# Kernel optimization log

Measured on AMD Instinct MI355X. Metric: run time of the kernel, lower is better.

The kernel has to match this reference:

```python
import jax, jax.numpy as jnp
import numpy as np

T = 2048        # sequence length
E = 1024        # embedding_dim
H = 1024        # hidden_dim
V = 50257       # vocab_size
TAGS = 50       # tagset_size


def setup_inputs() -> dict:
    key = jax.random.key(0)
    ks = jax.random.split(key, 8)
    s = 1.0 / np.sqrt(H)
    return {
        "sentence": jax.random.randint(ks[0], (T,), 0, V, dtype=jnp.int64),
        "emb": jax.random.normal(ks[1], (V, E), dtype=jnp.float32),
        "W_ih": jax.random.uniform(ks[2], (3 * H, E), jnp.float32, -s, s),
        "W_hh": jax.random.uniform(ks[3], (3 * H, H), jnp.float32, -s, s),
        "b_ih": jax.random.uniform(ks[4], (3 * H,), jnp.float32, -s, s),
        "b_hh": jax.random.uniform(ks[5], (3 * H,), jnp.float32, -s, s),
        "W_out": jax.random.uniform(ks[6], (TAGS, H), jnp.float32, -s, s),
        "b_out": jax.random.uniform(ks[7], (TAGS,), jnp.float32, -s, s),
    }


def _gru_scan(x, W_ih, W_hh, b_ih, b_hh):
    # x: [T, E]. Precompute all input-side gate projections in one GEMM.
    gi_all = x @ W_ih.T + b_ih            # [T, 3H]
    W_hhT = W_hh.T                         # [H, 3H]
    h0 = jnp.zeros((W_hh.shape[1],), x.dtype)

    def step(h, gi):
        gh = h @ W_hhT + b_hh              # [3H]
        i_r, i_z, i_n = jnp.split(gi, 3)
        h_r, h_z, h_n = jnp.split(gh, 3)
        r = jax.nn.sigmoid(i_r + h_r)
        z = jax.nn.sigmoid(i_z + h_z)
        n = jnp.tanh(i_n + r * h_n)
        h_new = (1.0 - z) * n + z * h
        return h_new, h_new

    _, hs = jax.lax.scan(step, h0, gi_all)  # hs: [T, H]
    return hs


def reference(sentence, emb, W_ih, W_hh, b_ih, b_hh, W_out, b_out):
    x = emb[sentence]                       # [T, E] embedding lookup
    hs = _gru_scan(x, W_ih, W_hh, b_ih, b_hh)  # [T, H]
    tag_space = hs @ W_out.T + b_out        # [T, TAGS]
    return jax.nn.log_softmax(tag_space, axis=-1)
```

## Files before the change

### kernel.cpp

```cpp
#include <hip/hip_runtime.h>
#include <hip/hip_bf16.h>


#define T_SEQ 2048
#define E_DIM 1024
#define H_DIM 1024
#define N3H   3072
#define VTAGS 50
#define VOCAB 50257
#define NWG   64
#define IPW   (H_DIM / NWG)
#define SBLK  512

typedef short bf16x8 __attribute__((ext_vector_type(8)));
typedef float f32x4  __attribute__((ext_vector_type(4)));
typedef unsigned int u32x4v __attribute__((ext_vector_type(4)));

__device__ inline unsigned short f2bf_rne(float f) {
  unsigned int u = __float_as_uint(f);
  u += 0x7FFFu + ((u >> 16) & 1u);
  return (unsigned short)(u >> 16);
}

__global__ __launch_bounds__(256) void k_gather_cast(
    const int* __restrict__ sent, const float* __restrict__ emb,
    unsigned short* __restrict__ Xb) {
  const int t = blockIdx.x;
  int row = sent[t];
  row = (row < 0) ? 0 : ((row >= VOCAB) ? VOCAB - 1 : row);
  const float4* src = (const float4*)(emb + (size_t)row * E_DIM);
  float4 v = src[threadIdx.x];
  ushort4 o;
  o.x = f2bf_rne(v.x); o.y = f2bf_rne(v.y); o.z = f2bf_rne(v.z); o.w = f2bf_rne(v.w);
  ((ushort4*)(Xb + (size_t)t * E_DIM))[threadIdx.x] = o;
}

__global__ __launch_bounds__(256) void k_cast_w(
    const float* __restrict__ W, unsigned short* __restrict__ Wb) {
  const int r = blockIdx.x;
  const float4* src = (const float4*)(W + (size_t)r * E_DIM);
  float4 v = src[threadIdx.x];
  ushort4 o;
  o.x = f2bf_rne(v.x); o.y = f2bf_rne(v.y); o.z = f2bf_rne(v.z); o.w = f2bf_rne(v.w);
  ((ushort4*)(Wb + (size_t)r * E_DIM))[threadIdx.x] = o;
}

__global__ __launch_bounds__(256) void k_gemm_gi(
    const unsigned short* __restrict__ Xb, const unsigned short* __restrict__ Wb,
    const float* __restrict__ b_ih, float* __restrict__ gi) {
  const int tid = threadIdx.x;
  const int lane = tid & 63;
  const int wv = tid >> 6;
  const int m_base = blockIdx.y * 128 + (wv & 1) * 64;
  const int n_base = blockIdx.x * 128 + (wv >> 1) * 64;
  const int lr = lane & 15;
  const int kq = (lane >> 4) * 8;
  f32x4 acc[4][4] = {};
  for (int k0 = 0; k0 < E_DIM; k0 += 32) {
    bf16x8 a[4], b[4];
#pragma unroll
    for (int mi = 0; mi < 4; ++mi)
      a[mi] = *(const bf16x8*)(Xb + (size_t)(m_base + mi * 16 + lr) * E_DIM + k0 + kq);
#pragma unroll
    for (int ni = 0; ni < 4; ++ni)
      b[ni] = *(const bf16x8*)(Wb + (size_t)(n_base + ni * 16 + lr) * E_DIM + k0 + kq);
#pragma unroll
    for (int mi = 0; mi < 4; ++mi)
#pragma unroll
      for (int ni = 0; ni < 4; ++ni)
        acc[mi][ni] = __builtin_amdgcn_mfma_f32_16x16x32_bf16(a[mi], b[ni], acc[mi][ni], 0, 0, 0);
  }
  const int row_q = (lane >> 4) * 4;
#pragma unroll
  for (int mi = 0; mi < 4; ++mi) {
#pragma unroll
    for (int ni = 0; ni < 4; ++ni) {
      const int col  = n_base + ni * 16 + lr;
      const int row0 = m_base + mi * 16 + row_q;
      const float bv = b_ih[col];
#pragma unroll
      for (int rr = 0; rr < 4; ++rr)
        gi[(size_t)(row0 + rr) * N3H + col] = acc[mi][ni][rr] + bv;
    }
  }
}

__global__ __launch_bounds__(SBLK) __attribute__((amdgpu_waves_per_eu(2, 2)))
void k_gru_scan(const float* __restrict__ W_hh, const float* __restrict__ b_hh,
                const float* __restrict__ gi, float* __restrict__ hs,
                unsigned long long* mb) {
  const int wg  = blockIdx.x;
  const int tid = threadIdx.x;
  const int row = tid >> 5;
  const int cg  = tid & 31;
  const int i   = wg * IPW + row;

  __shared__ float hsh[2][H_DIM];

  f32x4 w0[8], w1[8], w2[8];
  {
    const f32x4* p0 = (const f32x4*)(W_hh + (size_t)i * H_DIM);
    const f32x4* p1 = (const f32x4*)(W_hh + (size_t)(H_DIM + i) * H_DIM);
    const f32x4* p2 = (const f32x4*)(W_hh + (size_t)(2 * H_DIM + i) * H_DIM);
#pragma unroll
    for (int q = 0; q < 8; ++q) {
      w0[q] = p0[cg + q * 32];
      w1[q] = p1[cg + q * 32];
      w2[q] = p2[cg + q * 32];
      asm volatile("" : "+v"(w0[q]), "+v"(w1[q]), "+v"(w2[q]));
    }
  }
  const float bh0 = b_hh[i], bh1 = b_hh[H_DIM + i], bh2 = b_hh[2 * H_DIM + i];

  for (int t = 0; t < T_SEQ; ++t) {
    const float gir = gi[(size_t)t * N3H + i];
    const float giz = gi[(size_t)t * N3H + H_DIM + i];
    const float gin = gi[(size_t)t * N3H + 2 * H_DIM + i];

    {
      const unsigned long long* pb = mb + (size_t)(t & 1) * H_DIM + tid * 2;
      const unsigned tt = (unsigned)t;
      u32x4v p;
      int it = 0;
      while (true) {
        asm volatile("global_load_dwordx4 %0, %1, off sc0 sc1\n\ts_waitcnt vmcnt(0)"
                     : "=v"(p) : "v"(pb));
        if (__all((p[1] == tt) & (p[3] == tt)) || ++it > (1 << 16)) break;
      }
      *(float2*)&hsh[t & 1][tid * 2] =
          make_float2(__uint_as_float(p[0]), __uint_as_float(p[2]));
    }
    __syncthreads();

    const float* hb = hsh[t & 1];
    const f32x4* hb4 = (const f32x4*)hb;
    float a0 = 0.f, a1 = 0.f, a2 = 0.f;
#pragma unroll
    for (int q = 0; q < 8; ++q) {
      f32x4 hv = hb4[cg + q * 32];
      a0 = fmaf(w0[q][0], hv[0], a0); a0 = fmaf(w0[q][1], hv[1], a0);
      a0 = fmaf(w0[q][2], hv[2], a0); a0 = fmaf(w0[q][3], hv[3], a0);
      a1 = fmaf(w1[q][0], hv[0], a1); a1 = fmaf(w1[q][1], hv[1], a1);
      a1 = fmaf(w1[q][2], hv[2], a1); a1 = fmaf(w1[q][3], hv[3], a1);
      a2 = fmaf(w2[q][0], hv[0], a2); a2 = fmaf(w2[q][1], hv[1], a2);
      a2 = fmaf(w2[q][2], hv[2], a2); a2 = fmaf(w2[q][3], hv[3], a2);
    }
#pragma unroll
    for (int off = 16; off >= 1; off >>= 1) {
      a0 += __shfl_xor(a0, off, 64);
      a1 += __shfl_xor(a1, off, 64);
      a2 += __shfl_xor(a2, off, 64);
    }
    const float r = 1.f / (1.f + __expf(-(gir + a0 + bh0)));
    const float z = 1.f / (1.f + __expf(-(giz + a1 + bh1)));
    const float nx = gin + r * (a2 + bh2);
    const float e2 = __expf(-2.f * fabsf(nx));
    float n = (1.f - e2) / (1.f + e2);
    n = (nx < 0.f) ? -n : n;
    const float hold = hb[i];
    const float hnew = (1.f - z) * n + z * hold;

    if (cg == 0) {
      const unsigned long long pack =
          ((unsigned long long)(unsigned)(t + 1) << 32) |
          (unsigned long long)__float_as_uint(hnew);
      __hip_atomic_store(&mb[(size_t)((t + 1) & 1) * H_DIM + i], pack,
                         __ATOMIC_RELAXED, __HIP_MEMORY_SCOPE_AGENT);
      hs[(size_t)t * H_DIM + i] = hnew;
    }
  }
}

__global__ __launch_bounds__(256) void k_out(
    const float* __restrict__ hs, const float* __restrict__ W_out,
    const float* __restrict__ b_out, float* __restrict__ out) {
  const int t = blockIdx.x;
  const int tid = threadIdx.x;
  const int wv = tid >> 6, lane = tid & 63;
  __shared__ float xs[H_DIM];
  __shared__ float tagv[64];
  ((float4*)xs)[tid] = ((const float4*)(hs + (size_t)t * H_DIM))[tid];
  __syncthreads();
  for (int g = wv; g < VTAGS; g += 4) {
    const float4* wr = (const float4*)(W_out + (size_t)g * H_DIM);
    const float4* xr = (const float4*)xs;
    float s = 0.f;
#pragma unroll
    for (int q = 0; q < 4; ++q) {
      float4 a = wr[lane * 4 + q];
      float4 b = xr[lane * 4 + q];
      s += a.x * b.x + a.y * b.y + a.z * b.z + a.w * b.w;
    }
#pragma unroll
    for (int off = 1; off < 64; off <<= 1) s += __shfl_xor(s, off, 64);
    if (lane == 0) tagv[g] = s + b_out[g];
  }
  __syncthreads();
  if (tid < 64) {
    const float v = (tid < VTAGS) ? tagv[tid] : -1e30f;
    float m = v;
#pragma unroll
    for (int off = 1; off < 64; off <<= 1) m = fmaxf(m, __shfl_xor(m, off, 64));
    float e = (tid < VTAGS) ? __expf(v - m) : 0.f;
    float se = e;
#pragma unroll
    for (int off = 1; off < 64; off <<= 1) se += __shfl_xor(se, off, 64);
    const float lse = logf(se);
    if (tid < VTAGS) out[(size_t)t * VTAGS + tid] = v - m - lse;
  }
}

extern "C" void kernel_launch(void* const* d_in, const int* in_sizes, int n_in,
                              void* d_out, int out_size, void* d_ws, size_t ws_size,
                              hipStream_t stream) {
  const int* sent    = (const int*)d_in[0];
  const float* emb   = (const float*)d_in[1];
  const float* W_ih  = (const float*)d_in[2];
  const float* W_hh  = (const float*)d_in[3];
  const float* b_ih  = (const float*)d_in[4];
  const float* b_hh  = (const float*)d_in[5];
  const float* W_out = (const float*)d_in[6];
  const float* b_out = (const float*)d_in[7];
  float* out = (float*)d_out;

  char* ws = (char*)d_ws;
  const size_t OFF_GI = 0;
  const size_t OFF_B  = (size_t)T_SEQ * N3H * 4;
  const size_t OFF_XB = OFF_B;
  const size_t OFF_WB = OFF_B + (size_t)T_SEQ * E_DIM * 2;
  const size_t OFF_HS = OFF_B;
  const size_t OFF_MB = OFF_B + 10485760;
  const size_t NEED = OFF_MB + 2 * H_DIM * 8;
  if (ws_size < NEED) return;

  float* gi = (float*)(ws + OFF_GI);
  unsigned short* Xb = (unsigned short*)(ws + OFF_XB);
  unsigned short* Wb = (unsigned short*)(ws + OFF_WB);
  float* hs = (float*)(ws + OFF_HS);
  unsigned long long* mb = (unsigned long long*)(ws + OFF_MB);

  hipMemsetAsync(mb, 0, 2 * H_DIM * 8, stream);

  k_gather_cast<<<T_SEQ, 256, 0, stream>>>(sent, emb, Xb);
  k_cast_w<<<N3H, 256, 0, stream>>>(W_ih, Wb);
  k_gemm_gi<<<dim3(N3H / 128, T_SEQ / 128), 256, 0, stream>>>(Xb, Wb, b_ih, gi);
  k_gru_scan<<<NWG, SBLK, 0, stream>>>(W_hh, b_hh, gi, hs, mb);
  k_out<<<T_SEQ, 256, 0, stream>>>(hs, W_out, b_out, out);
}
```

Measured before the change: 5.875 ms.

## Replace packed value-tag polling with per-workgroup flags plus separate data buffer

The GRU scan used to spin on an 8-byte (value, step-tag) pair for every hidden element, so each thread polled 16 bytes of the shared state. Now each workgroup stores its hidden values, hits a barrier, then publishes one step flag. Consumers spin only on 64 flags and afterwards load the 4 KB state vector once. This cuts the bytes polled per spin iteration, but it adds a workgroup barrier and a second dependent global load to every step. It also relies on relaxed stores being ordered across the barrier without an explicit release fence. The register-pinning asm is moved inside the time loop.

```diff
diff --git a/kernel.cpp b/kernel.cpp
--- a/kernel.cpp
+++ b/kernel.cpp
@@ -14,7 +14,7 @@
 
 typedef short bf16x8 __attribute__((ext_vector_type(8)));
 typedef float f32x4  __attribute__((ext_vector_type(4)));
-typedef unsigned int u32x4v __attribute__((ext_vector_type(4)));
+typedef float f32x2  __attribute__((ext_vector_type(2)));
 
 __device__ inline unsigned short f2bf_rne(float f) {
   unsigned int u = __float_as_uint(f);
@@ -88,11 +88,12 @@
 __global__ __launch_bounds__(SBLK) __attribute__((amdgpu_waves_per_eu(2, 2)))
 void k_gru_scan(const float* __restrict__ W_hh, const float* __restrict__ b_hh,
                 const float* __restrict__ gi, float* __restrict__ hs,
-                unsigned long long* mb) {
+                float* data, int* tags) {
   const int wg  = blockIdx.x;
   const int tid = threadIdx.x;
   const int row = tid >> 5;
   const int cg  = tid & 31;
+  const int lane = tid & 63;
   const int i   = wg * IPW + row;
 
   __shared__ float hsh[2][H_DIM];
@@ -107,28 +108,39 @@
       w0[q] = p0[cg + q * 32];
       w1[q] = p1[cg + q * 32];
       w2[q] = p2[cg + q * 32];
-      asm volatile("" : "+v"(w0[q]), "+v"(w1[q]), "+v"(w2[q]));
     }
   }
   const float bh0 = b_hh[i], bh1 = b_hh[H_DIM + i], bh2 = b_hh[2 * H_DIM + i];
 
   for (int t = 0; t < T_SEQ; ++t) {
+    asm volatile("" : "+v"(w0[0]), "+v"(w0[1]), "+v"(w0[2]), "+v"(w0[3]),
+                      "+v"(w0[4]), "+v"(w0[5]), "+v"(w0[6]), "+v"(w0[7]),
+                      "+v"(w1[0]), "+v"(w1[1]), "+v"(w1[2]), "+v"(w1[3]),
+                      "+v"(w1[4]), "+v"(w1[5]), "+v"(w1[6]), "+v"(w1[7]),
+                      "+v"(w2[0]), "+v"(w2[1]), "+v"(w2[2]), "+v"(w2[3]),
+                      "+v"(w2[4]), "+v"(w2[5]), "+v"(w2[6]), "+v"(w2[7]));
+
     const float gir = gi[(size_t)t * N3H + i];
     const float giz = gi[(size_t)t * N3H + H_DIM + i];
     const float gin = gi[(size_t)t * N3H + 2 * H_DIM + i];
 
     {
-      const unsigned long long* pb = mb + (size_t)(t & 1) * H_DIM + tid * 2;
+      const int* tp = tags + (size_t)(t & 1) * 64 + lane;
       const unsigned tt = (unsigned)t;
-      u32x4v p;
+      unsigned v;
       int it = 0;
       while (true) {
-        asm volatile("global_load_dwordx4 %0, %1, off sc0 sc1\n\ts_waitcnt vmcnt(0)"
-                     : "=v"(p) : "v"(pb));
-        if (__all((p[1] == tt) & (p[3] == tt)) || ++it > (1 << 16)) break;
+        asm volatile("global_load_dword %0, %1, off sc0 sc1\n\ts_waitcnt vmcnt(0)"
+                     : "=v"(v) : "v"(tp));
+        if (__all(v == tt) || ++it > (1 << 16)) break;
       }
-      *(float2*)&hsh[t & 1][tid * 2] =
-          make_float2(__uint_as_float(p[0]), __uint_as_float(p[2]));
+    }
+    {
+      const float* dp = data + (size_t)(t & 1) * H_DIM + tid * 2;
+      f32x2 d;
+      asm volatile("global_load_dwordx2 %0, %1, off sc0 sc1\n\ts_waitcnt vmcnt(0)"
+                   : "=v"(d) : "v"(dp));
+      *(f32x2*)&hsh[t & 1][tid * 2] = d;
     }
     __syncthreads();
 
@@ -161,13 +173,14 @@
     const float hnew = (1.f - z) * n + z * hold;
 
     if (cg == 0) {
-      const unsigned long long pack =
-          ((unsigned long long)(unsigned)(t + 1) << 32) |
-          (unsigned long long)__float_as_uint(hnew);
-      __hip_atomic_store(&mb[(size_t)((t + 1) & 1) * H_DIM + i], pack,
+      __hip_atomic_store(&data[(size_t)((t + 1) & 1) * H_DIM + i], hnew,
                          __ATOMIC_RELAXED, __HIP_MEMORY_SCOPE_AGENT);
       hs[(size_t)t * H_DIM + i] = hnew;
     }
+    __syncthreads();
+    if (tid == 0)
+      __hip_atomic_store(&tags[(size_t)((t + 1) & 1) * 64 + wg], t + 1,
+                         __ATOMIC_RELAXED, __HIP_MEMORY_SCOPE_AGENT);
   }
 }
 
@@ -229,21 +242,23 @@
   const size_t OFF_XB = OFF_B;
   const size_t OFF_WB = OFF_B + (size_t)T_SEQ * E_DIM * 2;
   const size_t OFF_HS = OFF_B;
-  const size_t OFF_MB = OFF_B + 10485760;
-  const size_t NEED = OFF_MB + 2 * H_DIM * 8;
+  const size_t OFF_DT = OFF_B + 10485760;
+  const size_t OFF_TG = OFF_DT + 2 * H_DIM * 4;
+  const size_t NEED = OFF_TG + 2 * 64 * 4;
   if (ws_size < NEED) return;
 
   float* gi = (float*)(ws + OFF_GI);
   unsigned short* Xb = (unsigned short*)(ws + OFF_XB);
   unsigned short* Wb = (unsigned short*)(ws + OFF_WB);
   float* hs = (float*)(ws + OFF_HS);
-  unsigned long long* mb = (unsigned long long*)(ws + OFF_MB);
-
-  hipMemsetAsync(mb, 0, 2 * H_DIM * 8, stream);
+  float* data = (float*)(ws + OFF_DT);
+  int* tags = (int*)(ws + OFF_TG);
+
+  hipMemsetAsync(ws + OFF_DT, 0, 2 * H_DIM * 4 + 2 * 64 * 4, stream);
 
   k_gather_cast<<<T_SEQ, 256, 0, stream>>>(sent, emb, Xb);
   k_cast_w<<<N3H, 256, 0, stream>>>(W_ih, Wb);
   k_gemm_gi<<<dim3(N3H / 128, T_SEQ / 128), 256, 0, stream>>>(Xb, Wb, b_ih, gi);
-  k_gru_scan<<<NWG, SBLK, 0, stream>>>(W_hh, b_hh, gi, hs, mb);
+  k_gru_scan<<<NWG, SBLK, 0, stream>>>(W_hh, b_hh, gi, hs, data, tags);
   k_out<<<T_SEQ, 256, 0, stream>>>(hs, W_out, b_out, out);
 }
```

After: 5.808 ms. No clear change (-1.1%).
